# Optimization experiments

Hardware: AMD Instinct MI355X
Metric: run time of the kernel (lower is better)

Reference implementation:

```python
import jax, jax.numpy as jnp
import numpy as np

B, N, QD = 2, 2048, 1024
HEADS, DIM_HEAD = 16, 64
INNER = HEADS * DIM_HEAD  # 1024
SCALE = DIM_HEAD ** -0.5


def setup_inputs() -> dict:
    key = jax.random.key(0)
    ks = jax.random.split(key, 8)
    x = jax.random.normal(ks[0], (B, N, QD), dtype=jnp.float32)
    bias = jax.random.normal(ks[1], (B, N, N), dtype=jnp.float32)
    mask = jax.random.randint(ks[2], (B, N), 0, 2) > 0
    # parameters (nn.Linear stores weight [out, in]; we keep [in, out] and matmul x @ W)
    Wq = jax.random.normal(ks[3], (QD, INNER), dtype=jnp.float32) * (QD ** -0.5)
    Wkv = jax.random.normal(ks[4], (QD, 2 * INNER), dtype=jnp.float32) * (QD ** -0.5)
    Wo = jax.random.normal(ks[5], (INNER, QD), dtype=jnp.float32) * (INNER ** -0.5)
    bo = jax.random.normal(ks[6], (QD,), dtype=jnp.float32) * 0.01
    return {"x": x, "bias": bias, "mask": mask, "Wq": Wq, "Wkv": Wkv, "Wo": Wo, "bo": bo}


def reference(x, bias, mask, Wq, Wkv, Wo, bo):
    b, n, _ = x.shape
    q = x @ Wq                      # [b, n, inner]
    kv = x @ Wkv                    # [b, n, 2*inner] (context defaults to x)
    k, v = jnp.split(kv, 2, axis=-1)
    # split heads: [b, h, n, d]
    split = lambda t: t.reshape(b, n, HEADS, DIM_HEAD).transpose(0, 2, 1, 3)
    q, k, v = split(q), split(k), split(v)
    sim = jnp.einsum('bhid,bhjd->bhij', q, k) * SCALE   # [b, h, n, n]
    sim = sim + bias[:, None, :, :]                      # additive bias broadcast over heads
    max_neg = -jnp.finfo(sim.dtype).max
    sim = jnp.where(mask[:, None, None, :], sim, max_neg)  # per-key mask
    attn = jax.nn.softmax(sim, axis=-1)
    out = jnp.einsum('bhij,bhjd->bhid', attn, v)         # [b, h, n, d]
    out = out.transpose(0, 2, 1, 3).reshape(b, n, INNER)  # merge heads
    return out @ Wo + bo
```

## Files before the change

kernel.cpp:

```cpp
#include <hip/hip_runtime.h>
#include <hip/hip_bf16.h>
#include <stdint.h>

#define B_     2
#define N_     2048
#define QD_    1024
#define H_     16
#define DH_    64
#define INNER_ 1024
#define SCALE_ 0.125f

typedef unsigned short u16;
typedef __attribute__((ext_vector_type(8))) short bf16x8;
typedef __attribute__((ext_vector_type(4))) float f32x4;
typedef __attribute__((ext_vector_type(4))) unsigned short u16x4;
typedef __attribute__((ext_vector_type(8))) unsigned short u16x8;

#define GLD16(gp, lp) __builtin_amdgcn_global_load_lds( \
    (const __attribute__((address_space(1))) unsigned int*)(gp), \
    (__attribute__((address_space(3))) unsigned int*)(lp), 16, 0, 0)

__device__ inline u16 f2bf(float f) {
    union { float f; uint32_t u; } c; c.f = f;
    uint32_t r = c.u + 0x7FFFu + ((c.u >> 16) & 1u);
    return (u16)(r >> 16);
}
__device__ inline float bf2f(u16 s) {
    union { uint32_t u; float f; } c; c.u = ((uint32_t)s) << 16;
    return c.f;
}
__device__ inline void split2(float v, u16 &h, u16 &l) {
    u16 hs = f2bf(v);
    h = hs;
    l = f2bf(v - bf2f(hs));
}
__device__ inline unsigned pk2(float a, float b) {
    float2 f; f.x = a; f.y = b;
    union { __hip_bfloat162 v; unsigned u; } c;
    c.v = __float22bfloat162_rn(f);
    return c.u;
}

__global__ __launch_bounds__(256) void prep_kernel(
    const float* __restrict__ x, u16* __restrict__ xh, u16* __restrict__ xl,
    const float* __restrict__ Wq, const float* __restrict__ Wkv, const float* __restrict__ Wo,
    u16* __restrict__ wTh, u16* __restrict__ wTl,
    u16* __restrict__ woTh, u16* __restrict__ woTl)
{
    __shared__ float t[32][33];
    const int blk = blockIdx.x, tid = threadIdx.x;
    if (blk < 4096) {
        int idx = blk * 256 + tid;
        float4 v = ((const float4*)x)[idx];
        u16x4 hv, lv; u16 h, l;
        split2(v.x, h, l); hv.x = h; lv.x = l;
        split2(v.y, h, l); hv.y = h; lv.y = l;
        split2(v.z, h, l); hv.z = h; lv.z = l;
        split2(v.w, h, l); hv.w = h; lv.w = l;
        ((u16x4*)xh)[idx] = hv;
        ((u16x4*)xl)[idx] = lv;
        return;
    }
    int local = blk - 4096;
    const float* src; u16 *dhi, *dlo; int C, bx, by;
    if (local < 1024)      { src = Wq;  dhi = wTh;                dlo = wTl;                C = 1024; by = local >> 5; bx = local & 31; }
    else if (local < 3072) { int l2 = local - 1024; src = Wkv; dhi = wTh + 1024 * 1024; dlo = wTl + 1024 * 1024; C = 2048; by = l2 >> 6; bx = l2 & 63; }
    else                   { int l2 = local - 3072; src = Wo;  dhi = woTh;               dlo = woTl;               C = 1024; by = l2 >> 5; bx = l2 & 31; }
    const int x0 = bx * 32, y0 = by * 32;
    const int tx = tid & 31, ty = tid >> 5;
    for (int yy = ty; yy < 32; yy += 8)
        t[yy][tx] = src[(size_t)(y0 + yy) * C + x0 + tx];
    __syncthreads();
    for (int i = ty; i < 32; i += 8) {
        float v = t[tx][i];
        u16 h, l; split2(v, h, l);
        size_t o = (size_t)(x0 + i) * 1024 + y0 + tx;
        dhi[o] = h; dlo[o] = l;
    }
}

__global__ __launch_bounds__(256) void gemm_qkv_bias(
    int mode,
    const u16* __restrict__ Ah, const u16* __restrict__ Al,
    const u16* __restrict__ Bh,
    u16* __restrict__ qh,
    u16* __restrict__ kb, u16* __restrict__ vT,
    const float* __restrict__ bias, const int* __restrict__ mask,
    u16* __restrict__ bsw)
{
    __shared__ __align__(16) char smem[49152];
    const int tid = threadIdx.x;

    int gid = -1, bid = -1;
    if (mode == 1) {
        if (blockIdx.x < 768) gid = blockIdx.x; else bid = blockIdx.x - 768;
    } else if (mode == 0) gid = blockIdx.x;
    else bid = blockIdx.x;

    if (bid >= 0) {
        float (*t)[65] = (float(*)[65])smem;
        const int b = bid >> 10, rest = bid & 1023;
        const int k0 = (rest & 31) * 64, q0 = (rest >> 5) * 64;
#pragma unroll
        for (int it = 0; it < 16; it++) {
            int idx = it * 256 + tid;
            int qq = idx >> 6, kk = idx & 63;
            t[qq][kk] = bias[((size_t)b * N_ + q0 + qq) * N_ + k0 + kk];
        }
        __syncthreads();
        const u16 NEG = f2bf(-1e30f);
        const int qt = q0 >> 6, jt = k0 >> 7, w0 = (k0 >> 5) & 3;
        const int p = tid >> 1, hf = tid & 1;
        const int wv = w0 + (p >> 6), lane = p & 63;
        const int quad = lane >> 4, l16 = lane & 15;
        const int kbase = (p >> 6) * 32 + quad * 8 + hf * 4;
        const int4 mv = *(const int4*)&mask[b * N_ + k0 + kbase];
        const int mok[4] = { mv.x, mv.y, mv.z, mv.w };
        u16x8 o0, o1;
#pragma unroll
        for (int i = 0; i < 8; i++) {
            int m = i >> 2, r = i & 3;
            o0[i] = mok[r] ? f2bf(t[m * 16 + l16][kbase + r]) : NEG;
        }
#pragma unroll
        for (int i = 0; i < 8; i++) {
            int m = 2 + (i >> 2), r = i & 3;
            o1[i] = mok[r] ? f2bf(t[m * 16 + l16][kbase + r]) : NEG;
        }
        size_t ob = ((((size_t)b * 32 + qt) * 16 + jt) * 4 + wv) * 2048
                    + (size_t)lane * 32 + hf * 16;
        *(u16x8*)&bsw[ob]     = o0;
        *(u16x8*)&bsw[ob + 8] = o1;
        return;
    }

    const int wave = tid >> 6, lane = tid & 63;
    const int quad = lane >> 4, l16 = lane & 15;
    const int wm = wave >> 1, wn = wave & 1;
    const int bx = gid % 24, by = gid / 24;
    const int bm = by * 128, bn = bx * 128;
    const bool comp = (bx < 8);

    f32x4 acc[4][4];
#pragma unroll
    for (int i = 0; i < 4; i++)
#pragma unroll
        for (int j = 0; j < 4; j++) acc[i][j] = (f32x4){0.f, 0.f, 0.f, 0.f};

    const int row0 = tid >> 2, g4 = tid & 3;
    const int r1 = row0, r2 = row0 + 64;
    const int gc1 = (g4 ^ (r1 & 3)) * 8, gc2 = (g4 ^ (r2 & 3)) * 8;
    const size_t a1 = (size_t)(bm + r1) * 1024 + gc1, a2 = (size_t)(bm + r2) * 1024 + gc2;
    const size_t b1 = (size_t)(bn + r1) * 1024 + gc1, b2 = (size_t)(bn + r2) * 1024 + gc2;
    const int ldsw = wave * 1024;

    auto issue = [&](char* base, int kn) {
        GLD16(Ah + a1 + kn, base + ldsw);
        GLD16(Ah + a2 + kn, base + 4096 + ldsw);
        GLD16(Bh + b1 + kn, base + 16384 + ldsw);
        GLD16(Bh + b2 + kn, base + 20480 + ldsw);
        if (comp) {
            GLD16(Al + a1 + kn, base + 8192 + ldsw);
            GLD16(Al + a2 + kn, base + 12288 + ldsw);
        }
    };

    issue(smem, 0);
    int cur = 0;
    for (int k0 = 0; k0 < 1024; k0 += 32) {
        __syncthreads();
        char* cb_ = smem + cur * 24576;
        if (k0 + 32 < 1024) issue(smem + (cur ^ 1) * 24576, k0 + 32);
        const u16* cAh = (const u16*)cb_;
        const u16* cAl = (const u16*)(cb_ + 8192);
        const u16* cBh = (const u16*)(cb_ + 16384);
        bf16x8 fah[4], fal[4], fbh[4];
#pragma unroll
        for (int s = 0; s < 4; s++) {
            int ra = wm * 64 + s * 16 + l16;
            int rb = wn * 64 + s * 16 + l16;
            int ca = (quad ^ (ra & 3)) * 8;
            int cb = (quad ^ (rb & 3)) * 8;
            fah[s] = *(const bf16x8*)&cAh[ra * 32 + ca];
            fbh[s] = *(const bf16x8*)&cBh[rb * 32 + cb];
            if (comp) fal[s] = *(const bf16x8*)&cAl[ra * 32 + ca];
        }
#pragma unroll
        for (int sm = 0; sm < 4; sm++)
#pragma unroll
            for (int sn = 0; sn < 4; sn++) {
                acc[sm][sn] = __builtin_amdgcn_mfma_f32_16x16x32_bf16(fah[sm], fbh[sn], acc[sm][sn], 0, 0, 0);
                if (comp)
                    acc[sm][sn] = __builtin_amdgcn_mfma_f32_16x16x32_bf16(fal[sm], fbh[sn], acc[sm][sn], 0, 0, 0);
            }
        cur ^= 1;
    }
#pragma unroll
    for (int sm = 0; sm < 4; sm++) {
        int rowb = bm + wm * 64 + sm * 16 + quad * 4;
        int bb = rowb >> 11, i0 = rowb & 2047;
#pragma unroll
        for (int sn = 0; sn < 4; sn++) {
            int col = bn + wn * 64 + sn * 16 + l16;
            int region = col >> 10;
            int hh = (col >> 6) & 15;
            int d = col & 63;
            if (region == 0) {
#pragma unroll
                for (int r = 0; r < 4; r++) {
                    size_t o = (((size_t)(bb * H_ + hh)) * N_ + i0 + r) * DH_ + d;
                    qh[o] = f2bf(acc[sm][sn][r] * SCALE_);
                }
            } else if (region == 1) {
#pragma unroll
                for (int r = 0; r < 4; r++) {
                    size_t o = (((size_t)(bb * H_ + hh)) * N_ + i0 + r) * DH_ + d;
                    kb[o] = f2bf(acc[sm][sn][r]);
                }
            } else {
                u16x4 pv;
#pragma unroll
                for (int r = 0; r < 4; r++) pv[r] = f2bf(acc[sm][sn][r]);
                *(u16x4*)&vT[(((size_t)(bb * H_ + hh)) * DH_ + d) * N_ + i0] = pv;
            }
        }
    }
}

__global__ __launch_bounds__(256) void gemm_out(
    const u16* __restrict__ Ab,
    const u16* __restrict__ Bh,
    const float* __restrict__ bo, float* __restrict__ out)
{
    __shared__ __align__(16) char smem[24576];
    const int tid = threadIdx.x;
    const int wave = tid >> 6, lane = tid & 63;
    const int quad = lane >> 4, l16 = lane & 15;
    const int wm = wave >> 1, wn = wave & 1;
    const int bm = blockIdx.y * 128, bn = blockIdx.x * 64;

    f32x4 acc[4][2];
#pragma unroll
    for (int i = 0; i < 4; i++)
#pragma unroll
        for (int j = 0; j < 2; j++) acc[i][j] = (f32x4){0.f, 0.f, 0.f, 0.f};

    const int row0 = tid >> 2, g4 = tid & 3;
    const int r1 = row0, r2 = row0 + 64;
    const int gc1 = (g4 ^ (r1 & 3)) * 8, gc2 = (g4 ^ (r2 & 3)) * 8;
    const size_t a1 = (size_t)(bm + r1) * 1024 + gc1, a2 = (size_t)(bm + r2) * 1024 + gc2;
    const size_t bgo = (size_t)(bn + r1) * 1024 + gc1;
    const int ldsw = wave * 1024;

    auto issue = [&](char* base, int kn) {
        GLD16(Ab + a1 + kn, base + ldsw);
        GLD16(Ab + a2 + kn, base + 4096 + ldsw);
        GLD16(Bh + bgo + kn, base + 8192 + ldsw);
    };

    issue(smem, 0);
    int cur = 0;
    for (int k0 = 0; k0 < 1024; k0 += 32) {
        __syncthreads();
        char* cb_ = smem + cur * 12288;
        if (k0 + 32 < 1024) issue(smem + (cur ^ 1) * 12288, k0 + 32);
        const u16* cA  = (const u16*)cb_;
        const u16* cBh = (const u16*)(cb_ + 8192);
        bf16x8 fa[4], fbh[2];
#pragma unroll
        for (int s = 0; s < 4; s++) {
            int ra = wm * 64 + s * 16 + l16;
            int ca = (quad ^ (ra & 3)) * 8;
            fa[s] = *(const bf16x8*)&cA[ra * 32 + ca];
        }
#pragma unroll
        for (int s = 0; s < 2; s++) {
            int rb = wn * 32 + s * 16 + l16;
            int cb = (quad ^ (rb & 3)) * 8;
            fbh[s] = *(const bf16x8*)&cBh[rb * 32 + cb];
        }
#pragma unroll
        for (int sm = 0; sm < 4; sm++)
#pragma unroll
            for (int sn = 0; sn < 2; sn++)
                acc[sm][sn] = __builtin_amdgcn_mfma_f32_16x16x32_bf16(fa[sm], fbh[sn], acc[sm][sn], 0, 0, 0);
        cur ^= 1;
    }
#pragma unroll
    for (int sm = 0; sm < 4; sm++) {
        int rowb = bm + wm * 64 + sm * 16 + quad * 4;
#pragma unroll
        for (int sn = 0; sn < 2; sn++) {
            int col = bn + wn * 32 + sn * 16 + l16;
            float bv = bo[col];
#pragma unroll
            for (int r = 0; r < 4; r++)
                out[(size_t)(rowb + r) * 1024 + col] = acc[sm][sn][r] + bv;
        }
    }
}

#define LDK 72
#define LDV 128

__global__ __launch_bounds__(256, 2) void attn_kernel(
    const u16* __restrict__ qh,
    const u16* __restrict__ kb, const u16* __restrict__ vT,
    const u16* __restrict__ bsw, u16* __restrict__ ob)
{
    __shared__ __align__(16) char smem[35328];
    u16* sK  = (u16*)smem;
    u16* sVt = (u16*)(smem + 18432);
    float* rO = (float*)smem;
    float* rL = (float*)(smem + 34816);

    const int bh = blockIdx.y, b = bh >> 4, h = bh & 15;
    const int qt = blockIdx.x, qbase = qt * 64;
    const int tid = threadIdx.x, wave = tid >> 6, lane = tid & 63;
    const int quad = lane >> 4, l16 = lane & 15;

    bf16x8 aq[4][2];
#pragma unroll
    for (int m = 0; m < 4; m++) {
        size_t qo = ((size_t)bh * N_ + qbase + m * 16 + l16) * DH_ + quad * 8;
        aq[m][0] = *(const bf16x8*)&qh[qo];
        aq[m][1] = *(const bf16x8*)&qh[qo + 32];
    }
    f32x4 Oacc[4][4], lacc[4];
#pragma unroll
    for (int m = 0; m < 4; m++) {
        lacc[m] = (f32x4){0.f, 0.f, 0.f, 0.f};
#pragma unroll
        for (int nd = 0; nd < 4; nd++) Oacc[m][nd] = (f32x4){0.f, 0.f, 0.f, 0.f};
    }
    bf16x8 ones;
#pragma unroll
    for (int i = 0; i < 8; i++) ones[i] = (short)0x3F80;

    const int rK = tid >> 3, cK = (tid & 7) * 8;
    const int sigK = ((rK & 4) << 2) + ((rK >> 3) << 2) + (rK & 3);
    const int rV = tid >> 4;
    const int vg = tid & 15;
    const int cV = vg * 8;
    const int vsw = (vg ^ (rV & 7)) * 8;
    const int vrg = ((wave * 4 + quad) ^ (l16 & 7)) * 8;
    const size_t kgbase = (size_t)bh * N_ * DH_;
    const size_t vgbase = (size_t)bh * DH_ * N_;
    const size_t bswb = (size_t)(b * 32 + qt) * 131072 + (size_t)wave * 2048
                        + (size_t)lane * 32;

    bf16x8 pK[4], pV[4];
    u16x8 cB[4], nB[4];
#pragma unroll
    for (int it = 0; it < 4; it++) {
        pK[it] = *(const bf16x8*)&kb[kgbase + (size_t)(rK + it * 32) * DH_ + cK];
        pV[it] = *(const bf16x8*)&vT[vgbase + (size_t)(rV + it * 16) * N_ + cV];
    }
#pragma unroll
    for (int c = 0; c < 4; c++) cB[c] = *(const u16x8*)&bsw[bswb + c * 8];

    for (int jt = 0; jt < 16; jt++) {
#pragma unroll
        for (int it = 0; it < 4; it++) {
            *(bf16x8*)&sK[(it * 32 + sigK) * LDK + cK] = pK[it];
            *(bf16x8*)&sVt[(rV + it * 16) * LDV + vsw] = pV[it];
        }
        __syncthreads();
        {
            int jn = (jt + 1) & 15;
            int j0n = jn * 128;
#pragma unroll
            for (int it = 0; it < 4; it++) {
                pK[it] = *(const bf16x8*)&kb[kgbase + (size_t)(j0n + rK + it * 32) * DH_ + cK];
                pV[it] = *(const bf16x8*)&vT[vgbase + (size_t)(rV + it * 16) * N_ + j0n + cV];
            }
            size_t bb = bswb + (size_t)jn * 8192;
#pragma unroll
            for (int c = 0; c < 4; c++) nB[c] = *(const u16x8*)&bsw[bb + c * 8];
        }
        bf16x8 kf[2][2], vf[4];
#pragma unroll
        for (int n = 0; n < 2; n++)
#pragma unroll
            for (int s = 0; s < 2; s++)
                kf[n][s] = *(const bf16x8*)&sK[(wave * 32 + n * 16 + l16) * LDK + s * 32 + quad * 8];
#pragma unroll
        for (int nd = 0; nd < 4; nd++)
            vf[nd] = *(const bf16x8*)&sVt[(nd * 16 + l16) * LDV + vrg];

#pragma unroll
        for (int m = 0; m < 4; m++) {
            f32x4 S0 = (f32x4){0.f, 0.f, 0.f, 0.f};
            f32x4 S1 = (f32x4){0.f, 0.f, 0.f, 0.f};
#pragma unroll
            for (int s = 0; s < 2; s++) {
                S0 = __builtin_amdgcn_mfma_f32_16x16x32_bf16(kf[0][s], aq[m][s], S0, 0, 0, 0);
                S1 = __builtin_amdgcn_mfma_f32_16x16x32_bf16(kf[1][s], aq[m][s], S1, 0, 0, 0);
            }
            float p0[4], p1[4];
#pragma unroll
            for (int r = 0; r < 4; r++) {
                p0[r] = __expf(S0[r] + bf2f(cB[m >> 1][(m & 1) * 4 + r]));
                p1[r] = __expf(S1[r] + bf2f(cB[2 + (m >> 1)][(m & 1) * 4 + r]));
            }
            union { bf16x8 v; unsigned w[4]; } pa;
            pa.w[0] = pk2(p0[0], p0[1]);
            pa.w[1] = pk2(p0[2], p0[3]);
            pa.w[2] = pk2(p1[0], p1[1]);
            pa.w[3] = pk2(p1[2], p1[3]);
            lacc[m] = __builtin_amdgcn_mfma_f32_16x16x32_bf16(pa.v, ones, lacc[m], 0, 0, 0);
#pragma unroll
            for (int nd = 0; nd < 4; nd++)
                Oacc[m][nd] = __builtin_amdgcn_mfma_f32_16x16x32_bf16(pa.v, vf[nd], Oacc[m][nd], 0, 0, 0);
        }
#pragma unroll
        for (int c = 0; c < 4; c++) cB[c] = nB[c];
        __syncthreads();
    }

    if (wave >= 2) {
        int slot = wave - 2;
#pragma unroll
        for (int m = 0; m < 4; m++) {
#pragma unroll
            for (int nd = 0; nd < 4; nd++)
#pragma unroll
                for (int r = 0; r < 4; r++)
                    rO[(slot * 64 + m * 16 + quad * 4 + r) * 68 + nd * 16 + l16] = Oacc[m][nd][r];
            if (l16 == 0)
#pragma unroll
                for (int r = 0; r < 4; r++)
                    rL[slot * 64 + m * 16 + quad * 4 + r] = lacc[m][r];
        }
    }
    __syncthreads();
    if (wave < 2) {
        int slot = wave;
#pragma unroll
        for (int m = 0; m < 4; m++) {
#pragma unroll
            for (int nd = 0; nd < 4; nd++)
#pragma unroll
                for (int r = 0; r < 4; r++) {
                    int idx = (slot * 64 + m * 16 + quad * 4 + r) * 68 + nd * 16 + l16;
                    rO[idx] += Oacc[m][nd][r];
                }
            if (l16 == 0)
#pragma unroll
                for (int r = 0; r < 4; r++)
                    rL[slot * 64 + m * 16 + quad * 4 + r] += lacc[m][r];
        }
    }
    __syncthreads();
    {
        const int q = tid >> 2, dg = (tid & 3) * 16;
        float l = rL[q] + rL[64 + q];
        float inv = 1.f / l;
        f32x4 s[4];
#pragma unroll
        for (int i4 = 0; i4 < 4; i4++) {
            s[i4] = *(const f32x4*)&rO[(size_t)q * 68 + dg + i4 * 4];
            f32x4 v = *(const f32x4*)&rO[(size_t)(64 + q) * 68 + dg + i4 * 4];
            s[i4] += v;
        }
        size_t obase = ((size_t)b * N_ + qbase + q) * INNER_ + h * 64 + dg;
#pragma unroll
        for (int i4 = 0; i4 < 4; i4++) {
            u16x4 o4;
#pragma unroll
            for (int r = 0; r < 4; r++) o4[r] = f2bf(s[i4][r] * inv);
            *(u16x4*)&ob[obase + i4 * 4] = o4;
        }
    }
}

extern "C" void kernel_launch(void* const* d_in, const int* in_sizes, int n_in,
                              void* d_out, int out_size, void* d_ws, size_t ws_size,
                              hipStream_t stream)
{
    const float* x    = (const float*)d_in[0];
    const float* bias = (const float*)d_in[1];
    const int*   mask = (const int*)d_in[2];
    const float* Wq   = (const float*)d_in[3];
    const float* Wkv  = (const float*)d_in[4];
    const float* Wo   = (const float*)d_in[5];
    const float* bo   = (const float*)d_in[6];
    float* out = (float*)d_out;

    char* w = (char*)d_ws;
    const size_t MB = 1024 * 1024;
    u16* q_h   = (u16*)(w);
    u16* k_b   = (u16*)(w + 16 * MB);
    u16* v_T   = (u16*)(w + 24 * MB);
    u16* xs_h  = (u16*)(w + 32 * MB);
    u16* xs_l  = (u16*)(w + 40 * MB);
    u16* wT_h  = (u16*)(w + 48 * MB);
    u16* wT_l  = (u16*)(w + 54 * MB);
    u16* woT_h = (u16*)(w + 60 * MB);
    u16* woT_l = (u16*)(w + 62 * MB);
    u16* o_b   = (u16*)(w + 64 * MB);

    const size_t bsw_bytes = (size_t)2 * N_ * N_ * sizeof(u16);
    const bool concurrent = ws_size >= 72 * MB + bsw_bytes;

    prep_kernel<<<8192, 256, 0, stream>>>(x, xs_h, xs_l, Wq, Wkv, Wo, wT_h, wT_l, woT_h, woT_l);

    if (concurrent) {
        u16* bsw = (u16*)(w + 72 * MB);
        gemm_qkv_bias<<<2816, 256, 0, stream>>>(1, xs_h, xs_l, wT_h,
                                                q_h, k_b, v_T, bias, mask, bsw);
        attn_kernel<<<dim3(32, 32), 256, 0, stream>>>(q_h, k_b, v_T, bsw, o_b);
    } else {
        u16* bsw = (u16*)(w + 32 * MB);
        gemm_qkv_bias<<<768, 256, 0, stream>>>(0, xs_h, xs_l, wT_h,
                                               q_h, k_b, v_T, bias, mask, bsw);
        gemm_qkv_bias<<<2048, 256, 0, stream>>>(2, xs_h, xs_l, wT_h,
                                                q_h, k_b, v_T, bias, mask, bsw);
        attn_kernel<<<dim3(32, 32), 256, 0, stream>>>(q_h, k_b, v_T, bsw, o_b);
    }
    gemm_out<<<dim3(16, 32), 256, 0, stream>>>(o_b, woT_h, bo, out);
}
```

Measured before the change: 251.0 us.

## Interleave bias swizzle into QKV GEMM mainloop and load attention K/V directly to registers

The separate bias-swizzle blocks are folded into the 768 QKV GEMM blocks. Each block reads bias and mask into registers at fixed k-steps and writes the swizzled bf16 bias a few steps later, so the bias traffic overlaps the GEMM instead of running as extra blocks. The attention kernel drops the LDS staging of K and V and the per-tile barriers. Each wave loads its own K/V MFMA fragments straight from global memory with register double-buffering and a fully unrolled loop. This trades LDS reuse and coalescing for more global loads per wave and higher register pressure.

New measurement: 287.0 us. 14.3% more time.

```diff
diff --git a/kernel.cpp b/kernel.cpp
--- a/kernel.cpp
+++ b/kernel.cpp
@@ -39,6 +39,9 @@
     union { __hip_bfloat162 v; unsigned u; } c;
     c.v = __float22bfloat162_rn(f);
     return c.u;
+}
+__device__ inline float f4get(const float4& v, int r) {
+    return r == 0 ? v.x : r == 1 ? v.y : r == 2 ? v.z : v.w;
 }
 
 __global__ __launch_bounds__(256) void prep_kernel(
@@ -79,6 +82,45 @@
     }
 }
 
+__device__ inline void bias_read(int T, int bkoff, int bl16,
+                                 const float* __restrict__ bias,
+                                 const int* __restrict__ mask,
+                                 float4 bR[4], int4& bM)
+{
+    int bb2 = T >> 10, rest = T & 1023;
+    int k0b = (rest & 31) * 64, q0 = (rest >> 5) * 64;
+    int kk = k0b + bkoff;
+    bM = *(const int4*)&mask[bb2 * N_ + kk];
+#pragma unroll
+    for (int m = 0; m < 4; m++)
+        bR[m] = *(const float4*)&bias[((size_t)bb2 * N_ + q0 + m * 16 + bl16) * N_ + kk];
+}
+__device__ inline void bias_store(int T, int bwvr, int blane, int bhf,
+                                  const float4 bR[4], const int4& bM,
+                                  u16* __restrict__ bsw)
+{
+    int bb2 = T >> 10, rest = T & 1023;
+    int k0b = (rest & 31) * 64, q0 = (rest >> 5) * 64;
+    int wv = ((k0b >> 5) & 3) + bwvr;
+    const u16 NEG = f2bf(-1e30f);
+    const int mok[4] = { bM.x, bM.y, bM.z, bM.w };
+    u16x8 o0, o1;
+#pragma unroll
+    for (int i = 0; i < 8; i++) {
+        int m = i >> 2, r = i & 3;
+        o0[i] = mok[r] ? f2bf(f4get(bR[m], r)) : NEG;
+    }
+#pragma unroll
+    for (int i = 0; i < 8; i++) {
+        int m = 2 + (i >> 2), r = i & 3;
+        o1[i] = mok[r] ? f2bf(f4get(bR[m], r)) : NEG;
+    }
+    size_t ob = ((((size_t)bb2 * 32 + (q0 >> 6)) * 16 + (k0b >> 7)) * 4 + wv) * 2048
+                + (size_t)blane * 32 + bhf * 16;
+    *(u16x8*)&bsw[ob]     = o0;
+    *(u16x8*)&bsw[ob + 8] = o1;
+}
+
 __global__ __launch_bounds__(256) void gemm_qkv_bias(
     int mode,
     const u16* __restrict__ Ah, const u16* __restrict__ Al,
@@ -91,48 +133,18 @@
     __shared__ __align__(16) char smem[49152];
     const int tid = threadIdx.x;
 
-    int gid = -1, bid = -1;
-    if (mode == 1) {
-        if (blockIdx.x < 768) gid = blockIdx.x; else bid = blockIdx.x - 768;
-    } else if (mode == 0) gid = blockIdx.x;
-    else bid = blockIdx.x;
-
-    if (bid >= 0) {
-        float (*t)[65] = (float(*)[65])smem;
-        const int b = bid >> 10, rest = bid & 1023;
-        const int k0 = (rest & 31) * 64, q0 = (rest >> 5) * 64;
-#pragma unroll
-        for (int it = 0; it < 16; it++) {
-            int idx = it * 256 + tid;
-            int qq = idx >> 6, kk = idx & 63;
-            t[qq][kk] = bias[((size_t)b * N_ + q0 + qq) * N_ + k0 + kk];
-        }
-        __syncthreads();
-        const u16 NEG = f2bf(-1e30f);
-        const int qt = q0 >> 6, jt = k0 >> 7, w0 = (k0 >> 5) & 3;
-        const int p = tid >> 1, hf = tid & 1;
-        const int wv = w0 + (p >> 6), lane = p & 63;
-        const int quad = lane >> 4, l16 = lane & 15;
-        const int kbase = (p >> 6) * 32 + quad * 8 + hf * 4;
-        const int4 mv = *(const int4*)&mask[b * N_ + k0 + kbase];
-        const int mok[4] = { mv.x, mv.y, mv.z, mv.w };
-        u16x8 o0, o1;
-#pragma unroll
-        for (int i = 0; i < 8; i++) {
-            int m = i >> 2, r = i & 3;
-            o0[i] = mok[r] ? f2bf(t[m * 16 + l16][kbase + r]) : NEG;
-        }
-#pragma unroll
-        for (int i = 0; i < 8; i++) {
-            int m = 2 + (i >> 2), r = i & 3;
-            o1[i] = mok[r] ? f2bf(t[m * 16 + l16][kbase + r]) : NEG;
-        }
-        size_t ob = ((((size_t)b * 32 + qt) * 16 + jt) * 4 + wv) * 2048
-                    + (size_t)lane * 32 + hf * 16;
-        *(u16x8*)&bsw[ob]     = o0;
-        *(u16x8*)&bsw[ob + 8] = o1;
+    if (mode == 2) {
+        const int bid = blockIdx.x;
+        const int bp = tid >> 1, bhf = tid & 1;
+        const int blane = bp & 63, bquad = blane >> 4, bl16 = blane & 15;
+        const int bwvr = bp >> 6;
+        const int bkoff = bwvr * 32 + bquad * 8 + bhf * 4;
+        float4 bR[4]; int4 bM;
+        bias_read(bid, bkoff, bl16, bias, mask, bR, bM);
+        bias_store(bid, bwvr, blane, bhf, bR, bM, bsw);
         return;
     }
+    const int gid = blockIdx.x;
 
     const int wave = tid >> 6, lane = tid & 63;
     const int quad = lane >> 4, l16 = lane & 15;
@@ -165,12 +177,27 @@
         }
     };
 
+    const int bp = tid >> 1, bhf = tid & 1;
+    const int blane = bp & 63, bquad = blane >> 4, bl16 = blane & 15;
+    const int bwvr = bp >> 6;
+    const int bkoff = bwvr * 32 + bquad * 8 + bhf * 4;
+    float4 bR[4]; int4 bM;
+
     issue(smem, 0);
     int cur = 0;
     for (int k0 = 0; k0 < 1024; k0 += 32) {
         __syncthreads();
         char* cb_ = smem + cur * 24576;
         if (k0 + 32 < 1024) issue(smem + (cur ^ 1) * 24576, k0 + 32);
+        if (mode == 1) {
+            const int kstep = k0 >> 5;
+            if (kstep == 3)  bias_read (gid,        bkoff, bl16, bias, mask, bR, bM);
+            if (kstep == 7)  bias_store(gid,        bwvr, blane, bhf, bR, bM, bsw);
+            if (kstep == 11) bias_read (gid + 768,  bkoff, bl16, bias, mask, bR, bM);
+            if (kstep == 15) bias_store(gid + 768,  bwvr, blane, bhf, bR, bM, bsw);
+            if (kstep == 19 && gid < 512) bias_read (gid + 1536, bkoff, bl16, bias, mask, bR, bM);
+            if (kstep == 23 && gid < 512) bias_store(gid + 1536, bwvr, blane, bhf, bR, bM, bsw);
+        }
         const u16* cAh = (const u16*)cb_;
         const u16* cAl = (const u16*)(cb_ + 8192);
         const u16* cBh = (const u16*)(cb_ + 16384);
@@ -300,17 +327,12 @@
     }
 }
 
-#define LDK 72
-#define LDV 128
-
 __global__ __launch_bounds__(256, 2) void attn_kernel(
     const u16* __restrict__ qh,
     const u16* __restrict__ kb, const u16* __restrict__ vT,
     const u16* __restrict__ bsw, u16* __restrict__ ob)
 {
     __shared__ __align__(16) char smem[35328];
-    u16* sK  = (u16*)smem;
-    u16* sVt = (u16*)(smem + 18432);
     float* rO = (float*)smem;
     float* rL = (float*)(smem + 34816);
 
@@ -337,65 +359,50 @@
 #pragma unroll
     for (int i = 0; i < 8; i++) ones[i] = (short)0x3F80;
 
-    const int rK = tid >> 3, cK = (tid & 7) * 8;
-    const int sigK = ((rK & 4) << 2) + ((rK >> 3) << 2) + (rK & 3);
-    const int rV = tid >> 4;
-    const int vg = tid & 15;
-    const int cV = vg * 8;
-    const int vsw = (vg ^ (rV & 7)) * 8;
-    const int vrg = ((wave * 4 + quad) ^ (l16 & 7)) * 8;
-    const size_t kgbase = (size_t)bh * N_ * DH_;
-    const size_t vgbase = (size_t)bh * DH_ * N_;
+    const int kperm = (l16 >> 2) * 8 + (l16 & 3);
+    const size_t kbase0 = ((size_t)bh * N_ + wave * 32 + kperm) * DH_ + quad * 8;
+    const size_t vbase0 = ((size_t)bh * DH_ + l16) * N_ + (wave * 4 + quad) * 8;
     const size_t bswb = (size_t)(b * 32 + qt) * 131072 + (size_t)wave * 2048
                         + (size_t)lane * 32;
 
-    bf16x8 pK[4], pV[4];
-    u16x8 cB[4], nB[4];
-#pragma unroll
-    for (int it = 0; it < 4; it++) {
-        pK[it] = *(const bf16x8*)&kb[kgbase + (size_t)(rK + it * 32) * DH_ + cK];
-        pV[it] = *(const bf16x8*)&vT[vgbase + (size_t)(rV + it * 16) * N_ + cV];
-    }
+    bf16x8 kc[2][2], vc[4];
+    u16x8 cB[4];
+#pragma unroll
+    for (int n = 0; n < 2; n++)
+#pragma unroll
+        for (int s = 0; s < 2; s++)
+            kc[n][s] = *(const bf16x8*)&kb[kbase0 + (size_t)(n * 4) * DH_ + s * 32];
+#pragma unroll
+    for (int nd = 0; nd < 4; nd++)
+        vc[nd] = *(const bf16x8*)&vT[vbase0 + (size_t)(nd * 16) * N_];
 #pragma unroll
     for (int c = 0; c < 4; c++) cB[c] = *(const u16x8*)&bsw[bswb + c * 8];
 
+#pragma unroll
     for (int jt = 0; jt < 16; jt++) {
-#pragma unroll
-        for (int it = 0; it < 4; it++) {
-            *(bf16x8*)&sK[(it * 32 + sigK) * LDK + cK] = pK[it];
-            *(bf16x8*)&sVt[(rV + it * 16) * LDV + vsw] = pV[it];
-        }
-        __syncthreads();
-        {
-            int jn = (jt + 1) & 15;
-            int j0n = jn * 128;
-#pragma unroll
-            for (int it = 0; it < 4; it++) {
-                pK[it] = *(const bf16x8*)&kb[kgbase + (size_t)(j0n + rK + it * 32) * DH_ + cK];
-                pV[it] = *(const bf16x8*)&vT[vgbase + (size_t)(rV + it * 16) * N_ + j0n + cV];
-            }
-            size_t bb = bswb + (size_t)jn * 8192;
+        bf16x8 kn_[2][2], vn_[4]; u16x8 nB[4];
+        if (jt < 15) {
+            int j0n = (jt + 1) * 128;
+#pragma unroll
+            for (int n = 0; n < 2; n++)
+#pragma unroll
+                for (int s = 0; s < 2; s++)
+                    kn_[n][s] = *(const bf16x8*)&kb[kbase0 + (size_t)(j0n + n * 4) * DH_ + s * 32];
+#pragma unroll
+            for (int nd = 0; nd < 4; nd++)
+                vn_[nd] = *(const bf16x8*)&vT[vbase0 + (size_t)(nd * 16) * N_ + j0n];
+            size_t bb = bswb + (size_t)(jt + 1) * 8192;
 #pragma unroll
             for (int c = 0; c < 4; c++) nB[c] = *(const u16x8*)&bsw[bb + c * 8];
         }
-        bf16x8 kf[2][2], vf[4];
-#pragma unroll
-        for (int n = 0; n < 2; n++)
-#pragma unroll
-            for (int s = 0; s < 2; s++)
-                kf[n][s] = *(const bf16x8*)&sK[(wave * 32 + n * 16 + l16) * LDK + s * 32 + quad * 8];
-#pragma unroll
-        for (int nd = 0; nd < 4; nd++)
-            vf[nd] = *(const bf16x8*)&sVt[(nd * 16 + l16) * LDV + vrg];
-
 #pragma unroll
         for (int m = 0; m < 4; m++) {
             f32x4 S0 = (f32x4){0.f, 0.f, 0.f, 0.f};
             f32x4 S1 = (f32x4){0.f, 0.f, 0.f, 0.f};
 #pragma unroll
             for (int s = 0; s < 2; s++) {
-                S0 = __builtin_amdgcn_mfma_f32_16x16x32_bf16(kf[0][s], aq[m][s], S0, 0, 0, 0);
-                S1 = __builtin_amdgcn_mfma_f32_16x16x32_bf16(kf[1][s], aq[m][s], S1, 0, 0, 0);
+                S0 = __builtin_amdgcn_mfma_f32_16x16x32_bf16(kc[0][s], aq[m][s], S0, 0, 0, 0);
+                S1 = __builtin_amdgcn_mfma_f32_16x16x32_bf16(kc[1][s], aq[m][s], S1, 0, 0, 0);
             }
             float p0[4], p1[4];
 #pragma unroll
@@ -411,11 +418,18 @@
             lacc[m] = __builtin_amdgcn_mfma_f32_16x16x32_bf16(pa.v, ones, lacc[m], 0, 0, 0);
 #pragma unroll
             for (int nd = 0; nd < 4; nd++)
-                Oacc[m][nd] = __builtin_amdgcn_mfma_f32_16x16x32_bf16(pa.v, vf[nd], Oacc[m][nd], 0, 0, 0);
-        }
-#pragma unroll
-        for (int c = 0; c < 4; c++) cB[c] = nB[c];
-        __syncthreads();
+                Oacc[m][nd] = __builtin_amdgcn_mfma_f32_16x16x32_bf16(pa.v, vc[nd], Oacc[m][nd], 0, 0, 0);
+        }
+        if (jt < 15) {
+#pragma unroll
+            for (int n = 0; n < 2; n++)
+#pragma unroll
+                for (int s = 0; s < 2; s++) kc[n][s] = kn_[n][s];
+#pragma unroll
+            for (int nd = 0; nd < 4; nd++) vc[nd] = vn_[nd];
+#pragma unroll
+            for (int c = 0; c < 4; c++) cB[c] = nB[c];
+        }
     }
 
     if (wave >= 2) {
@@ -507,8 +521,8 @@
 
     if (concurrent) {
         u16* bsw = (u16*)(w + 72 * MB);
-        gemm_qkv_bias<<<2816, 256, 0, stream>>>(1, xs_h, xs_l, wT_h,
-                                                q_h, k_b, v_T, bias, mask, bsw);
+        gemm_qkv_bias<<<768, 256, 0, stream>>>(1, xs_h, xs_l, wT_h,
+                                               q_h, k_b, v_T, bias, mask, bsw);
         attn_kernel<<<dim3(32, 32), 256, 0, stream>>>(q_h, k_b, v_T, bsw, o_b);
     } else {
         u16* bsw = (u16*)(w + 32 * MB);
```
